# Kernel tuning notes

Hardware: AMD Instinct MI355X
Metric: run time of the kernel (lower is better)

The kernel has to match this reference:

```python
import jax, jax.numpy as jnp
import numpy as np


def setup_inputs() -> dict:
    key = jax.random.key(0)
    k1, k2, k3, k4 = jax.random.split(key, 4)
    B, L, K, E, V = 32, 256, 8, 768, 50000
    hidden_feature = jax.random.normal(k1, (B, L, E), dtype=jnp.float32)
    similar_words_sent = jax.random.randint(k2, (B, L, K), 0, V, dtype=jnp.int64)
    word2vec = jax.random.normal(k3, (V, E), dtype=jnp.float32)
    # xavier_uniform for (E, E)
    limit = float(np.sqrt(6.0 / (E + E)))
    weight = jax.random.uniform(k4, (E, E), dtype=jnp.float32, minval=-limit, maxval=limit)
    return {
        "hidden_feature": hidden_feature,
        "similar_words_sent": similar_words_sent,
        "word2vec": word2vec,
        "weight": weight,
    }


def reference(hidden_feature, similar_words_sent, word2vec, weight):
    # Gather k similar-word embeddings: [B, L, K, E]
    k_sims = word2vec[similar_words_sent]
    # Bilinear attention scores: (q @ W) . k  -> [B, L, K]
    q_proj = jnp.einsum("ble,ef->blf", hidden_feature, weight)
    scores = jnp.einsum("ble,blke->blk", q_proj, k_sims)
    attn = jax.nn.softmax(scores, axis=-1)
    # Dropout is identity in eval / rate 0.
    out = jnp.einsum("blk,blke->ble", attn, k_sims)
    return out
```

## Files before the change

### kernel.cpp

```cpp
#include <hip/hip_runtime.h>
#include <hip/hip_bf16.h>


typedef __attribute__((ext_vector_type(8))) _Float16 f16x8;
typedef __attribute__((ext_vector_type(4))) float f32x4;

__device__ __forceinline__ unsigned short f2h(float f) {
    _Float16 h = (_Float16)f;
    return __builtin_bit_cast(unsigned short, h);
}
__device__ __forceinline__ float h2f(unsigned short u) {
    return (float)__builtin_bit_cast(_Float16, u);
}

__device__ __forceinline__ void gload16(const void* g, void* l) {
    __builtin_amdgcn_global_load_lds(
        (const __attribute__((address_space(1))) unsigned int*)g,
        (__attribute__((address_space(3))) unsigned int*)l, 16, 0, 0);
}

__global__ __launch_bounds__(256) void split_all(const float4* __restrict__ x,
                                                 ushort4* __restrict__ hf, int n4,
                                                 const float* __restrict__ W,
                                                 unsigned short* __restrict__ WfT,
                                                 int K, int N, int ablocks) {
    __shared__ float tile[32][33];
    if ((int)blockIdx.x < ablocks) {
        int i = blockIdx.x * 256 + threadIdx.x;
        const int stride = ablocks * 256;
        for (; i < n4; i += stride) {
            float4 v = x[i];
            ushort4 h;
            h.x = f2h(v.x); h.y = f2h(v.y); h.z = f2h(v.z); h.w = f2h(v.w);
            hf[i] = h;
        }
    } else {
        const int bid = blockIdx.x - ablocks;
        const int nbk = K / 32;
        const int bk = (bid % nbk) * 32, bn = (bid / nbk) * 32;
        const int tx = threadIdx.x & 31, ty = threadIdx.x >> 5;
#pragma unroll
        for (int r = ty; r < 32; r += 8)
            tile[r][tx] = W[(size_t)(bk + r) * N + bn + tx];
        __syncthreads();
#pragma unroll
        for (int r = ty; r < 32; r += 8) {
            float v = tile[tx][r];
            WfT[(size_t)(bn + r) * K + bk + tx] = f2h(v);
        }
    }
}


#define BM 128
#define BN 64
#define BK 64

__global__ __launch_bounds__(256) void gemm_mfma_f16(
        const unsigned short* __restrict__ Af, const unsigned short* __restrict__ BfT,
        unsigned short* __restrict__ C, int M, int N, int K) {

    const int nwg = gridDim.x;
    const int per = nwg >> 3;
    const int l   = (blockIdx.x & 7) * per + (blockIdx.x >> 3);
    const int nbn = N / BN;
    const int bm  = (l / nbn) * BM;
    const int bn  = (l % nbn) * BN;

    __shared__ unsigned short lds[3 * 1536 * 8];
    const int BOFF = 1024;
    const int BUF  = 1536;

    const int tid  = threadIdx.x;
    const int lane = tid & 63;
    const int w    = tid >> 6;
    const int lr   = lane & 15, lg = lane >> 4;
    const int wm   = w >> 1, wn = w & 1;

    const int lane8 = lane >> 3;
    const int kcl   = (lane & 7) ^ lane8;

    f32x4 acc[4][2];
#pragma unroll
    for (int m = 0; m < 4; ++m)
#pragma unroll
        for (int n = 0; n < 2; ++n) acc[m][n] = (f32x4){0.f, 0.f, 0.f, 0.f};

    auto STAGE = [&](int k0, int buf) {
#pragma unroll
        for (int i = 0; i < 4; ++i) {
            size_t g = (size_t)(bm + 32 * w + 8 * i + lane8) * K + k0 + kcl * 8;
            gload16(Af + g, &lds[(size_t)(buf * BUF + 256 * w + 64 * i) * 8]);
        }
#pragma unroll
        for (int i = 0; i < 2; ++i) {
            size_t g = (size_t)(bn + 16 * w + 8 * i + lane8) * K + k0 + kcl * 8;
            gload16(BfT + g, &lds[(size_t)(buf * BUF + BOFF + 128 * w + 64 * i) * 8]);
        }
    };

    const int niter = K / BK;
    STAGE(0, 0);
    STAGE(BK, 1);
    int b0 = 0, b1 = 1, b2 = 2;

    for (int it = 0; it < niter; ++it) {
        if (it == niter - 1) asm volatile("s_waitcnt vmcnt(0)" ::: "memory");
        else                 asm volatile("s_waitcnt vmcnt(6)" ::: "memory");
        __builtin_amdgcn_s_barrier();
        if (it + 2 < niter) STAGE((it + 2) * BK, b2);

        const int base = b0 * BUF;
#pragma unroll
        for (int ks = 0; ks < 2; ++ks) {
            const int kc = ks * 4 + lg;
            const int kx = kc ^ (lr & 7);
            f16x8 a[4], b[2];
#pragma unroll
            for (int m = 0; m < 4; ++m) {
                int slot = base + (wm * 64 + m * 16 + lr) * 8 + kx;
                a[m] = *(const f16x8*)&lds[(size_t)slot * 8];
            }
#pragma unroll
            for (int n = 0; n < 2; ++n) {
                int slot = base + BOFF + (wn * 32 + n * 16 + lr) * 8 + kx;
                b[n] = *(const f16x8*)&lds[(size_t)slot * 8];
            }
#pragma unroll
            for (int m = 0; m < 4; ++m)
#pragma unroll
                for (int n = 0; n < 2; ++n)
                    acc[m][n] = __builtin_amdgcn_mfma_f32_16x16x32_f16(a[m], b[n], acc[m][n], 0, 0, 0);
        }
        int t = b0; b0 = b1; b1 = b2; b2 = t;
    }

#pragma unroll
    for (int m = 0; m < 4; ++m)
#pragma unroll
        for (int n = 0; n < 2; ++n) {
            const int col = bn + wn * 32 + n * 16 + lr;
            const int r0  = bm + wm * 64 + m * 16 + lg * 4;
#pragma unroll
            for (int j = 0; j < 4; ++j)
                C[(size_t)(r0 + j) * N + col] = f2h(acc[m][n][j]);
        }
}

__global__ __launch_bounds__(256) void attn_fused_h(
        const unsigned short* __restrict__ qf,
        const int* __restrict__ sws,
        const float* __restrict__ w2v,
        float* __restrict__ out) {
    const int wave = threadIdx.x >> 6;
    const int lane = threadIdx.x & 63;
    const size_t row = (size_t)blockIdx.x * 4 + wave;

    const ushort4* q4 = (const ushort4*)(qf + row * 768);
    float4 q[3];
#pragma unroll
    for (int j = 0; j < 3; ++j) {
        ushort4 h = q4[j * 64 + lane];
        q[j].x = h2f(h.x); q[j].y = h2f(h.y); q[j].z = h2f(h.z); q[j].w = h2f(h.w);
    }

    float4 ks[8][3];
    float dot[8];
#pragma unroll
    for (int k = 0; k < 8; ++k) {
        int id = sws[row * 8 + k];
        const float4* kp = (const float4*)(w2v + (size_t)id * 768);
        float d = 0.f;
#pragma unroll
        for (int j = 0; j < 3; ++j) {
            float4 v = kp[j * 64 + lane];
            ks[k][j] = v;
            d += q[j].x * v.x;
            d += q[j].y * v.y;
            d += q[j].z * v.z;
            d += q[j].w * v.w;
        }
        dot[k] = d;
    }
#pragma unroll
    for (int k = 0; k < 8; ++k) {
        float d = dot[k];
#pragma unroll
        for (int m = 1; m < 64; m <<= 1) d += __shfl_xor(d, m);
        dot[k] = d;
    }
    float mx = dot[0];
#pragma unroll
    for (int k = 1; k < 8; ++k) mx = fmaxf(mx, dot[k]);
    float wt[8];
    float s = 0.f;
#pragma unroll
    for (int k = 0; k < 8; ++k) { wt[k] = __expf(dot[k] - mx); s += wt[k]; }
    const float inv = 1.f / s;

    float4 o[3];
#pragma unroll
    for (int j = 0; j < 3; ++j) { o[j].x = 0.f; o[j].y = 0.f; o[j].z = 0.f; o[j].w = 0.f; }
#pragma unroll
    for (int k = 0; k < 8; ++k) {
        const float a = wt[k] * inv;
#pragma unroll
        for (int j = 0; j < 3; ++j) {
            o[j].x += a * ks[k][j].x;
            o[j].y += a * ks[k][j].y;
            o[j].z += a * ks[k][j].z;
            o[j].w += a * ks[k][j].w;
        }
    }
    float4* o4 = (float4*)(out + row * 768);
#pragma unroll
    for (int j = 0; j < 3; ++j) o4[j * 64 + lane] = o[j];
}

#define GM_BM 128
#define GM_BN 64
#define GM_BK 16
#define GM_TM 8
#define GM_TN 4

__global__ __launch_bounds__(256) void gemm_qproj(const float* __restrict__ A,
                                                  const float* __restrict__ B,
                                                  float* __restrict__ C,
                                                  int M, int N, int K) {
    __shared__ float As[GM_BK][GM_BM];
    __shared__ float Bs[GM_BK][GM_BN];
    const int tid = threadIdx.x;
    const int tx = tid & 15;
    const int ty = tid >> 4;
    const int bm = blockIdx.x * GM_BM;
    const int bn = blockIdx.y * GM_BN;
    float acc[GM_TM][GM_TN];
#pragma unroll
    for (int i = 0; i < GM_TM; ++i)
#pragma unroll
        for (int j = 0; j < GM_TN; ++j) acc[i][j] = 0.f;
    for (int k0 = 0; k0 < K; k0 += GM_BK) {
#pragma unroll
        for (int i = 0; i < 2; ++i) {
            int idx = tid * 2 + i;
            int row = idx >> 2;
            int c4  = idx & 3;
            float4 v = *(const float4*)(A + (size_t)(bm + row) * K + k0 + c4 * 4);
            As[c4 * 4 + 0][row] = v.x;
            As[c4 * 4 + 1][row] = v.y;
            As[c4 * 4 + 2][row] = v.z;
            As[c4 * 4 + 3][row] = v.w;
        }
        {
            int row = tid >> 4;
            int c4  = tid & 15;
            float4 v = *(const float4*)(B + (size_t)(k0 + row) * N + bn + c4 * 4);
            *(float4*)&Bs[row][c4 * 4] = v;
        }
        __syncthreads();
#pragma unroll
        for (int k = 0; k < GM_BK; ++k) {
            float a[GM_TM], b[GM_TN];
#pragma unroll
            for (int i = 0; i < GM_TM; ++i) a[i] = As[k][ty * GM_TM + i];
#pragma unroll
            for (int j = 0; j < GM_TN; ++j) b[j] = Bs[k][tx * GM_TN + j];
#pragma unroll
            for (int i = 0; i < GM_TM; ++i)
#pragma unroll
                for (int j = 0; j < GM_TN; ++j) acc[i][j] += a[i] * b[j];
        }
        __syncthreads();
    }
#pragma unroll
    for (int i = 0; i < GM_TM; ++i) {
        float4 v;
        v.x = acc[i][0]; v.y = acc[i][1]; v.z = acc[i][2]; v.w = acc[i][3];
        *(float4*)(C + (size_t)(bm + ty * GM_TM + i) * N + bn + tx * GM_TN) = v;
    }
}

__global__ __launch_bounds__(256) void attn_fused(const float* __restrict__ qproj,
                                                  const int* __restrict__ sws,
                                                  const float* __restrict__ w2v,
                                                  float* __restrict__ out) {
    const int wave = threadIdx.x >> 6;
    const int lane = threadIdx.x & 63;
    const size_t row = (size_t)blockIdx.x * 4 + wave;

    const float4* q4 = (const float4*)(qproj + row * 768);
    float4 q[3];
#pragma unroll
    for (int j = 0; j < 3; ++j) q[j] = q4[j * 64 + lane];

    float4 ks[8][3];
    float dot[8];
#pragma unroll
    for (int k = 0; k < 8; ++k) {
        int id = sws[row * 8 + k];
        const float4* kp = (const float4*)(w2v + (size_t)id * 768);
        float d = 0.f;
#pragma unroll
        for (int j = 0; j < 3; ++j) {
            float4 v = kp[j * 64 + lane];
            ks[k][j] = v;
            d += q[j].x * v.x + q[j].y * v.y + q[j].z * v.z + q[j].w * v.w;
        }
        dot[k] = d;
    }
#pragma unroll
    for (int k = 0; k < 8; ++k) {
        float d = dot[k];
#pragma unroll
        for (int m = 1; m < 64; m <<= 1) d += __shfl_xor(d, m);
        dot[k] = d;
    }
    float mx = dot[0];
#pragma unroll
    for (int k = 1; k < 8; ++k) mx = fmaxf(mx, dot[k]);
    float wq[8];
    float s = 0.f;
#pragma unroll
    for (int k = 0; k < 8; ++k) { wq[k] = __expf(dot[k] - mx); s += wq[k]; }
    const float inv = 1.f / s;

    float4 o[3];
#pragma unroll
    for (int j = 0; j < 3; ++j) { o[j].x = 0.f; o[j].y = 0.f; o[j].z = 0.f; o[j].w = 0.f; }
#pragma unroll
    for (int k = 0; k < 8; ++k) {
        const float a = wq[k] * inv;
#pragma unroll
        for (int j = 0; j < 3; ++j) {
            o[j].x += a * ks[k][j].x;
            o[j].y += a * ks[k][j].y;
            o[j].z += a * ks[k][j].z;
            o[j].w += a * ks[k][j].w;
        }
    }
    float4* o4 = (float4*)(out + row * 768);
#pragma unroll
    for (int j = 0; j < 3; ++j) o4[j * 64 + lane] = o[j];
}

extern "C" void kernel_launch(void* const* d_in, const int* in_sizes, int n_in,
                              void* d_out, int out_size, void* d_ws, size_t ws_size,
                              hipStream_t stream) {
    const float* hidden = (const float*)d_in[0];
    const int*   sws    = (const int*)d_in[1];
    const float* w2v    = (const float*)d_in[2];
    const float* weight = (const float*)d_in[3];
    float*       out    = (float*)d_out;

    const int E = 768;
    const int M = in_sizes[0] / E;

    const size_t szA = (size_t)M * E;
    const size_t szB = (size_t)E * E;
    const size_t need = (2 * szA + szB) * sizeof(unsigned short);

    if (ws_size >= need) {
        unsigned short* Af  = (unsigned short*)d_ws;
        unsigned short* WfT = Af + szA;
        unsigned short* Qf  = WfT + szB;

        const int ablocks = 2048;
        const int wblocks = (E / 32) * (E / 32);
        split_all<<<ablocks + wblocks, 256, 0, stream>>>(
            (const float4*)hidden, (ushort4*)Af, M * E / 4,
            weight, WfT, E, E, ablocks);

        dim3 ggrid((M / BM) * (E / BN));
        gemm_mfma_f16<<<ggrid, 256, 0, stream>>>(Af, WfT, Qf, M, E, E);

        attn_fused_h<<<dim3(M / 4), 256, 0, stream>>>(Qf, sws, w2v, out);
    } else {
        float* qproj = out;
        dim3 ggrid(M / GM_BM, E / GM_BN);
        gemm_qproj<<<ggrid, 256, 0, stream>>>(hidden, weight, qproj, M, E, E);
        attn_fused<<<dim3(M / 4), 256, 0, stream>>>(qproj, sws, w2v, out);
    }
}
```

Measured before the change: 64.70 us.

## Specialize GEMM to fixed shape with double buffering; pack gathered keys to fp16

The MFMA GEMM is specialized to compile-time K=N=768 with precomputed row pointers, and its triple-buffered pipeline with manual vmcnt waits becomes a double-buffered loop with a __syncthreads per iteration, which halves LDS use and may allow higher occupancy but gives less load/compute overlap. In the attention kernel the eight neighbour indices are read with two vector loads, and the gathered embeddings are held in registers as packed fp16 instead of fp32 to cut register pressure. That adds conversion instructions and rounds the weighted-sum inputs to half precision. The fast path is now restricted to M==8192.

After: 62.99 us. 1.03x faster.

```diff
diff --git a/kernel.cpp b/kernel.cpp
--- a/kernel.cpp
+++ b/kernel.cpp
@@ -55,19 +55,18 @@
 #define BM 128
 #define BN 64
 #define BK 64
+#define GEMM_K 768
+#define GEMM_N 768
 
 __global__ __launch_bounds__(256) void gemm_mfma_f16(
         const unsigned short* __restrict__ Af, const unsigned short* __restrict__ BfT,
-        unsigned short* __restrict__ C, int M, int N, int K) {
-
-    const int nwg = gridDim.x;
-    const int per = nwg >> 3;
-    const int l   = (blockIdx.x & 7) * per + (blockIdx.x >> 3);
-    const int nbn = N / BN;
-    const int bm  = (l / nbn) * BM;
-    const int bn  = (l % nbn) * BN;
-
-    __shared__ unsigned short lds[3 * 1536 * 8];
+        unsigned short* __restrict__ C) {
+
+    const int l   = (blockIdx.x & 7) * 96 + (blockIdx.x >> 3);
+    const int bm  = (l / 12) * BM;
+    const int bn  = (l % 12) * BN;
+
+    __shared__ unsigned short lds[2 * 1536 * 8];
     const int BOFF = 1024;
     const int BUF  = 1536;
 
@@ -86,31 +85,33 @@
 #pragma unroll
         for (int n = 0; n < 2; ++n) acc[m][n] = (f32x4){0.f, 0.f, 0.f, 0.f};
 
+    const unsigned short* aB[4];
+    const unsigned short* bB[2];
+#pragma unroll
+    for (int i = 0; i < 4; ++i)
+        aB[i] = Af + (size_t)(bm + 32 * w + 8 * i + lane8) * GEMM_K + kcl * 8;
+#pragma unroll
+    for (int i = 0; i < 2; ++i)
+        bB[i] = BfT + (size_t)(bn + 16 * w + 8 * i + lane8) * GEMM_K + kcl * 8;
+
     auto STAGE = [&](int k0, int buf) {
 #pragma unroll
-        for (int i = 0; i < 4; ++i) {
-            size_t g = (size_t)(bm + 32 * w + 8 * i + lane8) * K + k0 + kcl * 8;
-            gload16(Af + g, &lds[(size_t)(buf * BUF + 256 * w + 64 * i) * 8]);
-        }
-#pragma unroll
-        for (int i = 0; i < 2; ++i) {
-            size_t g = (size_t)(bn + 16 * w + 8 * i + lane8) * K + k0 + kcl * 8;
-            gload16(BfT + g, &lds[(size_t)(buf * BUF + BOFF + 128 * w + 64 * i) * 8]);
-        }
+        for (int i = 0; i < 4; ++i)
+            gload16(aB[i] + k0, &lds[(size_t)(buf * BUF + 256 * w + 64 * i) * 8]);
+#pragma unroll
+        for (int i = 0; i < 2; ++i)
+            gload16(bB[i] + k0, &lds[(size_t)(buf * BUF + BOFF + 128 * w + 64 * i) * 8]);
     };
 
-    const int niter = K / BK;
     STAGE(0, 0);
-    STAGE(BK, 1);
-    int b0 = 0, b1 = 1, b2 = 2;
-
-    for (int it = 0; it < niter; ++it) {
-        if (it == niter - 1) asm volatile("s_waitcnt vmcnt(0)" ::: "memory");
-        else                 asm volatile("s_waitcnt vmcnt(6)" ::: "memory");
-        __builtin_amdgcn_s_barrier();
-        if (it + 2 < niter) STAGE((it + 2) * BK, b2);
-
-        const int base = b0 * BUF;
+    __syncthreads();
+
+#pragma unroll
+    for (int it = 0; it < GEMM_K / BK; ++it) {
+        const int cur = it & 1;
+        if (it + 1 < GEMM_K / BK) STAGE((it + 1) * BK, cur ^ 1);
+
+        const int base = cur * BUF;
 #pragma unroll
         for (int ks = 0; ks < 2; ++ks) {
             const int kc = ks * 4 + lg;
@@ -132,7 +133,7 @@
                 for (int n = 0; n < 2; ++n)
                     acc[m][n] = __builtin_amdgcn_mfma_f32_16x16x32_f16(a[m], b[n], acc[m][n], 0, 0, 0);
         }
-        int t = b0; b0 = b1; b1 = b2; b2 = t;
+        __syncthreads();
     }
 
 #pragma unroll
@@ -143,7 +144,7 @@
             const int r0  = bm + wm * 64 + m * 16 + lg * 4;
 #pragma unroll
             for (int j = 0; j < 4; ++j)
-                C[(size_t)(r0 + j) * N + col] = f2h(acc[m][n][j]);
+                C[(size_t)(r0 + j) * GEMM_N + col] = f2h(acc[m][n][j]);
         }
 }
 
@@ -156,6 +157,10 @@
     const int lane = threadIdx.x & 63;
     const size_t row = (size_t)blockIdx.x * 4 + wave;
 
+    const int4 ia = *(const int4*)(sws + row * 8);
+    const int4 ib = *(const int4*)(sws + row * 8 + 4);
+    int id[8] = {ia.x, ia.y, ia.z, ia.w, ib.x, ib.y, ib.z, ib.w};
+
     const ushort4* q4 = (const ushort4*)(qf + row * 768);
     float4 q[3];
 #pragma unroll
@@ -164,21 +169,23 @@
         q[j].x = h2f(h.x); q[j].y = h2f(h.y); q[j].z = h2f(h.z); q[j].w = h2f(h.w);
     }
 
-    float4 ks[8][3];
+    uint2 kp16[8][3];
     float dot[8];
 #pragma unroll
     for (int k = 0; k < 8; ++k) {
-        int id = sws[row * 8 + k];
-        const float4* kp = (const float4*)(w2v + (size_t)id * 768);
+        const float4* kp = (const float4*)(w2v + (size_t)id[k] * 768);
         float d = 0.f;
 #pragma unroll
         for (int j = 0; j < 3; ++j) {
             float4 v = kp[j * 64 + lane];
-            ks[k][j] = v;
             d += q[j].x * v.x;
             d += q[j].y * v.y;
             d += q[j].z * v.z;
             d += q[j].w * v.w;
+            uint2 p;
+            p.x = (unsigned int)f2h(v.x) | ((unsigned int)f2h(v.y) << 16);
+            p.y = (unsigned int)f2h(v.z) | ((unsigned int)f2h(v.w) << 16);
+            kp16[k][j] = p;
         }
         dot[k] = d;
     }
@@ -206,10 +213,11 @@
         const float a = wt[k] * inv;
 #pragma unroll
         for (int j = 0; j < 3; ++j) {
-            o[j].x += a * ks[k][j].x;
-            o[j].y += a * ks[k][j].y;
-            o[j].z += a * ks[k][j].z;
-            o[j].w += a * ks[k][j].w;
+            uint2 p = kp16[k][j];
+            o[j].x += a * h2f((unsigned short)(p.x & 0xffff));
+            o[j].y += a * h2f((unsigned short)(p.x >> 16));
+            o[j].z += a * h2f((unsigned short)(p.y & 0xffff));
+            o[j].w += a * h2f((unsigned short)(p.y >> 16));
         }
     }
     float4* o4 = (float4*)(out + row * 768);
@@ -359,7 +367,7 @@
     const size_t szB = (size_t)E * E;
     const size_t need = (2 * szA + szB) * sizeof(unsigned short);
 
-    if (ws_size >= need) {
+    if (ws_size >= need && M == 8192) {
         unsigned short* Af  = (unsigned short*)d_ws;
         unsigned short* WfT = Af + szA;
         unsigned short* Qf  = WfT + szB;
@@ -371,7 +379,7 @@
             weight, WfT, E, E, ablocks);
 
         dim3 ggrid((M / BM) * (E / BN));
-        gemm_mfma_f16<<<ggrid, 256, 0, stream>>>(Af, WfT, Qf, M, E, E);
+        gemm_mfma_f16<<<ggrid, 256, 0, stream>>>(Af, WfT, Qf);
 
         attn_fused_h<<<dim3(M / 4), 256, 0, stream>>>(Qf, sws, w2v, out);
     } else {
```
